# Kernel tuning notes

Hardware: AMD Instinct MI355X
Metric: run time of the kernel (lower is better)

Reference implementation:

```python
import jax, jax.numpy as jnp
import numpy as np

N = 10000      # nodes
E = 320000     # edges (avg degree 32)
SI, VI = 256, 32   # node scalar / vector channels
SE, VE = 64, 4     # edge scalar / vector channels
SO, VO = 256, 32   # output channels
IN_S = 2 * SI + SE         # 576 (self_message=True)
IN_V = 2 * VI + VE         # 68
H = max(IN_V, VO)          # 68, GBP hidden vector dim
EPS = 1e-8


def setup_inputs() -> dict:
    key = jax.random.key(0)
    ks = jax.random.split(key, 9)
    node_s = jax.random.normal(ks[0], (N, SI), jnp.float32)
    node_v = jax.random.normal(ks[1], (N, VI, 3), jnp.float32)
    edge_s = jax.random.normal(ks[2], (E, SE), jnp.float32)
    edge_v = jax.random.normal(ks[3], (E, VE, 3), jnp.float32)
    # GBP params (stored as [in, out] so y = x @ W)
    wh = jax.random.normal(ks[4], (IN_V, H), jnp.float32) / np.sqrt(IN_V)
    ws_w = jax.random.normal(ks[5], (IN_S + H, SO), jnp.float32) / np.sqrt(IN_S + H)
    ws_b = jnp.zeros((SO,), jnp.float32)
    wv = jax.random.normal(ks[6], (H, VO), jnp.float32) / np.sqrt(H)
    edge_index = jax.random.randint(ks[7], (2, E), 0, N, jnp.int64)
    return {"node_s": node_s, "node_v": node_v, "edge_s": edge_s,
            "edge_v": edge_v, "wh": wh, "ws_w": ws_w, "ws_b": ws_b,
            "wv": wv, "edge_index": edge_index}


def reference(node_s, node_v, edge_s, edge_v, wh, ws_w, ws_b, wv, edge_index):
    n = node_s.shape[0]
    src, dst = edge_index[0], edge_index[1]
    # gather + tuple_cat((s_j, v_j), edge_attr, (s_i, v_i))
    s_cat = jnp.concatenate([node_s[src], edge_s, node_s[dst]], axis=-1)   # [E, IN_S]
    v_cat = jnp.concatenate([node_v[src], edge_v, node_v[dst]], axis=-2)   # [E, IN_V, 3]
    # GBP message (activations=(None,None), no vector gate)
    v_pre = jnp.swapaxes(v_cat, -1, -2)                # [E, 3, IN_V]
    vh = v_pre @ wh                                    # [E, 3, H]
    vn = jnp.sqrt(jnp.maximum(jnp.sum(vh * vh, axis=-2), EPS))  # _norm_no_nan, [E, H]
    s_msg = jnp.concatenate([s_cat, vn], axis=-1) @ ws_w + ws_b  # [E, SO]
    v_msg = jnp.swapaxes(vh @ wv, -1, -2)              # [E, VO, 3]
    # scatter-mean to target nodes
    agg_s = jax.ops.segment_sum(s_msg, dst, num_segments=n)       # [N, SO]
    agg_v = jax.ops.segment_sum(v_msg, dst, num_segments=n)       # [N, VO, 3]
    cnt = jax.ops.segment_sum(jnp.ones((s_msg.shape[0],), s_msg.dtype), dst,
                              num_segments=n)
    cnt = jnp.maximum(cnt, 1.0)
    out_s = agg_s / cnt[:, None]
    out_v = agg_v / cnt[:, None, None]
    # _merge(s, V): flatten vector channels and append to scalars
    return jnp.concatenate([out_s, out_v.reshape(n, 3 * VO)], axis=-1)  # [N, SO+3*VO]
```

## Files before the change

kernel.cpp:

```cpp
#include <hip/hip_runtime.h>
#include <hip/hip_bf16.h>

#define N_NODES 10000
#define E_TOT   320000

typedef __attribute__((ext_vector_type(8))) short short8;
typedef __attribute__((ext_vector_type(4))) short s16x4;
typedef __attribute__((ext_vector_type(4))) float f32x4;

#define HIST_OFF    0u
#define FILL_OFF    40000u
#define ZERO_BYTES  80000u
#define ROWPTR_OFF  80000u
#define PERM_OFF    120064u
#define PSRC_OFF    1400064u
#define PQ_OFF      2680064u
#define QV_OFF      12280064u
#define WHV4_OFF    14200064u
#define WBIG_OFF    14200576u
#define NSBF_OFF    14544640u
#define ANSB_OFF    19664640u
#define EAB_OFF     24784640u
#define AP_OFF      27984640u
#define AEV_OFF     36144640u
#define AGGV_OFF    36624640u
#define FLAGS_OFF   40464640u
#define NODES_OFF   120064u

union BfS { __hip_bfloat16 h; short s; };
__device__ __forceinline__ short f2bf(float x) { BfS u; u.h = __float2bfloat16(x); return u.s; }
__device__ __forceinline__ float bf(short x) { BfS u; u.s = x; return __bfloat162float(u.h); }
__device__ __forceinline__ float ldin(const void* p, int f32m, long i) {
  return f32m ? ((const float*)p)[i] : __bfloat162float(((const __hip_bfloat16*)p)[i]);
}
__device__ __forceinline__ int get_ei(const void* p, int i64m, long i) {
  return i64m ? (int)(((const long long*)p)[i]) : ((const int*)p)[i];
}

__global__ __launch_bounds__(256) void detect_kernel(
    const unsigned short* __restrict__ ns_u16,
    const int* __restrict__ ei_i32, int* __restrict__ flags)
{
  __shared__ int cf, ci;
  if (threadIdx.x == 0) { cf = 0; ci = 0; }
  __syncthreads();
  int c1 = 0;
  for (int i = threadIdx.x; i < 8192; i += 256) {
    unsigned e = (ns_u16[2 * i] >> 7) & 0xFF;
    if (e < 100 || e > 140) c1++;
  }
  int c2 = 0;
  for (int i = threadIdx.x; i < 4096; i += 256)
    if (ei_i32[2 * i + 1] != 0) c2++;
  atomicAdd(&cf, c1); atomicAdd(&ci, c2);
  __syncthreads();
  if (threadIdx.x == 0) {
    flags[0] = (cf > 512) ? 1 : 0;
    flags[1] = (ci < 100) ? 1 : 0;
  }
}

__global__ __launch_bounds__(256) void hist_kernel(
    const void* __restrict__ edge_index, const int* __restrict__ flags,
    int* __restrict__ hist)
{
  const int i64m = flags[1];
  int e = blockIdx.x * 256 + threadIdx.x;
  int dst = get_ei(edge_index, i64m, (long)E_TOT + e);
  atomicAdd(&hist[dst], 1);
}

__global__ __launch_bounds__(256) void scan_kernel(
    const int* __restrict__ hist, int* __restrict__ rowptr)
{
  __shared__ int part[256];
  int tid = threadIdx.x;
  int base = tid * 40;
  int s = 0;
  for (int i = 0; i < 40; ++i) { int idx = base + i; if (idx < N_NODES) s += hist[idx]; }
  part[tid] = s;
  __syncthreads();
  for (int off = 1; off < 256; off <<= 1) {
    int v = (tid >= off) ? part[tid - off] : 0;
    __syncthreads();
    part[tid] += v;
    __syncthreads();
  }
  int run = (tid > 0) ? part[tid - 1] : 0;
  for (int i = 0; i < 40; ++i) {
    int idx = base + i;
    if (idx < N_NODES) { rowptr[idx] = run; run += hist[idx]; }
  }
  if (tid == 255) rowptr[N_NODES] = run;
}

__global__ __launch_bounds__(256) void permute_kernel(
    const void* __restrict__ edge_index, const int* __restrict__ flags,
    const int* __restrict__ rowptr, int* __restrict__ fill,
    int* __restrict__ perm, int* __restrict__ psrc)
{
  const int i64m = flags[1];
  int e = blockIdx.x * 256 + threadIdx.x;
  int dst = get_ei(edge_index, i64m, (long)E_TOT + e);
  int src = get_ei(edge_index, i64m, e);
  int pos = rowptr[dst] + atomicAdd(&fill[dst], 1);
  perm[pos] = e; psrc[pos] = src;
}

__global__ __launch_bounds__(256) void prep_kernel(
    const void* __restrict__ ws_w, const void* __restrict__ wh,
    const void* __restrict__ wv, const int* __restrict__ flags,
    short* __restrict__ Wbig, float* __restrict__ whv4)
{
  const int f32m = flags[0];
  int b = blockIdx.x, tid = threadIdx.x;
  if (b < 672) {
    int flat = b * 256 + tid;
    int o = flat / 672, k = flat % 672;
    short v = 0;
    if (k < 320)      v = f2bf(ldin(ws_w, f32m, (long)k * 256 + o));
    else if (k < 388) v = f2bf(ldin(ws_w, f32m, (long)(576 + k - 320) * 256 + o));
    else if (k >= 416) v = f2bf(ldin(ws_w, f32m, (long)(k - 96) * 256 + o));
    Wbig[flat] = v;
  } else if (tid < 128) {
    int q = tid / 32, c = tid % 32;
    float acc = 0.f;
    for (int h = 0; h < 68; ++h)
      acc += ldin(wh, f32m, (32 + q) * 68 + h) * ldin(wv, f32m, h * 32 + c);
    whv4[tid] = acc;
  }
}

__global__ __launch_bounds__(256) void node_pre(
    const void* __restrict__ node_v, const void* __restrict__ wh,
    const void* __restrict__ wv, const void* __restrict__ node_s,
    const int* __restrict__ flags,
    short* __restrict__ PQ, short* __restrict__ QV, short* __restrict__ ns_bf)
{
  const int f32m = flags[0];
  int n0 = blockIdx.x * 4, tid = threadIdx.x;
  __shared__ float nv[4][96];
  __shared__ float pq[4][408];
  for (int i = tid; i < 4 * 96; i += 256) nv[i / 96][i % 96] = ldin(node_v, f32m, (long)n0 * 96 + i);
  for (int i = tid; i < 1024; i += 256)
    ns_bf[(long)n0 * 256 + i] = f2bf(ldin(node_s, f32m, (long)n0 * 256 + i));
  __syncthreads();
  for (int o = tid; o < 4 * 408; o += 256) {
    int i = o / 408, r0 = o % 408;
    int part = r0 / 204, r = r0 % 204, d = r / 68, h = r % 68;
    int cbase = part ? 36 : 0;
    float acc = 0.f;
#pragma unroll
    for (int c = 0; c < 32; ++c)
      acc += nv[i][c * 3 + d] * ldin(wh, f32m, (cbase + c) * 68 + h);
    pq[i][r0] = acc;
  }
  __syncthreads();
  for (int o = tid; o < 4 * 480; o += 256) {
    int i = o / 480, k = o % 480;
    short v = 0;
    if (k < 272) {
      int h = k >> 2, d = k & 3;
      if (d < 3) v = f2bf(pq[i][d * 68 + h]);
    } else if (k < 476) {
      v = f2bf(pq[i][204 + (k - 272)]);
    }
    PQ[(long)(n0 + i) * 480 + k] = v;
  }
  for (int o = tid; o < 4 * 96; o += 256) {
    int i = o / 96, r = o % 96, d = r / 32, c = r % 32;
    float acc = 0.f;
    for (int h = 0; h < 68; ++h)
      acc += pq[i][204 + d * 68 + h] * ldin(wv, f32m, h * 32 + c);
    QV[(long)(n0 + i) * 96 + r] = f2bf(acc);
  }
}

template <int F32M>
__device__ __forceinline__ void edge_body(
    const void* __restrict__ edge_v, const void* __restrict__ edge_s,
    const void* __restrict__ wh,
    const int* __restrict__ rowptr, const int* __restrict__ perm,
    const int* __restrict__ psrc, const short* __restrict__ PQ,
    const short* __restrict__ nsb,
    short* __restrict__ ANSb, short* __restrict__ EAb,
    float* __restrict__ AP, float* __restrict__ AEV)
{
  const int tid = threadIdx.x;
  const int lane = tid & 63, w = tid >> 6;
  const int n = blockIdx.x;
  const int beg = rowptr[n], deg = rowptr[n + 1] - beg;
  const bool has2 = (lane < 4);
  const int h2 = 64 + lane;
  const float w4a0 = ldin(wh, F32M, 32 * 68 + lane);
  const float w4a1 = ldin(wh, F32M, 33 * 68 + lane);
  const float w4a2 = ldin(wh, F32M, 34 * 68 + lane);
  const float w4a3 = ldin(wh, F32M, 35 * 68 + lane);
  const float w4b0 = has2 ? ldin(wh, F32M, 32 * 68 + h2) : 0.f;
  const float w4b1 = has2 ? ldin(wh, F32M, 33 * 68 + h2) : 0.f;
  const float w4b2 = has2 ? ldin(wh, F32M, 34 * 68 + h2) : 0.f;
  const float w4b3 = has2 ? ldin(wh, F32M, 35 * 68 + h2) : 0.f;
  const short* pqQ = PQ + (long)n * 480 + 272;
  const float qa0 = bf(pqQ[0 * 68 + lane]);
  const float qa1 = bf(pqQ[1 * 68 + lane]);
  const float qa2 = bf(pqQ[2 * 68 + lane]);
  const float qb0 = has2 ? bf(pqQ[0 * 68 + h2]) : 0.f;
  const float qb1 = has2 ? bf(pqQ[1 * 68 + h2]) : 0.f;
  const float qb2 = has2 ? bf(pqQ[2 * 68 + h2]) : 0.f;
  float an0 = 0.f, an1 = 0.f, an2 = 0.f, an3 = 0.f;
  float ap0 = 0.f, ap1 = 0.f, ap2 = 0.f;
  float bq0 = 0.f, bq1 = 0.f, bq2 = 0.f;
  float avna = 0.f, avnb = 0.f, aes = 0.f, aev = 0.f;
  int e = w;
  int sv = 0, eid = 0;
  if (e < deg) { sv = psrc[beg + e]; eid = perm[beg + e]; }
  while (e < deg) {
    int en = e + 4, svn = 0, eidn = 0;
    if (en < deg) { svn = psrc[beg + en]; eidn = perm[beg + en]; }
    float ev0, ev1, ev2, ev3, ev4, ev5, ev6, ev7, ev8, ev9, evA, evB;
    if (F32M) {
      const float* evp = (const float*)edge_v + (long)eid * 12;
      f32x4 a = *(const f32x4*)evp;
      f32x4 b = *(const f32x4*)(evp + 4);
      f32x4 c = *(const f32x4*)(evp + 8);
      ev0 = a.x; ev1 = a.y; ev2 = a.z; ev3 = a.w;
      ev4 = b.x; ev5 = b.y; ev6 = b.z; ev7 = b.w;
      ev8 = c.x; ev9 = c.y; evA = c.z; evB = c.w;
    } else {
      const short* evp = (const short*)edge_v + (long)eid * 12;
      s16x4 a = *(const s16x4*)evp;
      s16x4 b = *(const s16x4*)(evp + 4);
      s16x4 c = *(const s16x4*)(evp + 8);
      ev0 = bf(a.x); ev1 = bf(a.y); ev2 = bf(a.z); ev3 = bf(a.w);
      ev4 = bf(b.x); ev5 = bf(b.y); ev6 = bf(b.z); ev7 = bf(b.w);
      ev8 = bf(c.x); ev9 = bf(c.y); evA = bf(c.z); evB = bf(c.w);
    }
    const short* ps = PQ + (long)sv * 480;
    s16x4 pv = *(const s16x4*)(ps + lane * 4);
    const float pa0 = bf(pv.x), pa1 = bf(pv.y), pa2 = bf(pv.z);
    s16x4 nvv = *(const s16x4*)(nsb + (long)sv * 256 + lane * 4);
    an0 += bf(nvv.x); an1 += bf(nvv.y); an2 += bf(nvv.z); an3 += bf(nvv.w);
    aes += ldin(edge_s, F32M, (long)eid * 64 + lane);
    if (lane < 12) aev += ldin(edge_v, F32M, (long)eid * 12 + lane);
    float v0 = pa0 + qa0 + ev0 * w4a0 + ev3 * w4a1 + ev6 * w4a2 + ev9 * w4a3;
    float v1 = pa1 + qa1 + ev1 * w4a0 + ev4 * w4a1 + ev7 * w4a2 + evA * w4a3;
    float v2 = pa2 + qa2 + ev2 * w4a0 + ev5 * w4a1 + ev8 * w4a2 + evB * w4a3;
    avna += sqrtf(fmaxf(v0 * v0 + v1 * v1 + v2 * v2, 1e-8f));
    ap0 += pa0; ap1 += pa1; ap2 += pa2;
    if (has2) {
      s16x4 p2 = *(const s16x4*)(ps + h2 * 4);
      const float pb0 = bf(p2.x), pb1 = bf(p2.y), pb2 = bf(p2.z);
      float u0 = pb0 + qb0 + ev0 * w4b0 + ev3 * w4b1 + ev6 * w4b2 + ev9 * w4b3;
      float u1 = pb1 + qb1 + ev1 * w4b0 + ev4 * w4b1 + ev7 * w4b2 + evA * w4b3;
      float u2 = pb2 + qb2 + ev2 * w4b0 + ev5 * w4b1 + ev8 * w4b2 + evB * w4b3;
      avnb += sqrtf(fmaxf(u0 * u0 + u1 * u1 + u2 * u2, 1e-8f));
      bq0 += pb0; bq1 += pb1; bq2 += pb2;
    }
    e = en; sv = svn; eid = eidn;
  }
  __shared__ float ansL[4][256];
  __shared__ float apL[4][204];
  __shared__ float avnL[4][132];
  __shared__ float aesL[4][64];
  __shared__ float aevL[4][12];
  ansL[w][lane * 4 + 0] = an0; ansL[w][lane * 4 + 1] = an1;
  ansL[w][lane * 4 + 2] = an2; ansL[w][lane * 4 + 3] = an3;
  apL[w][lane * 3 + 0] = ap0; apL[w][lane * 3 + 1] = ap1; apL[w][lane * 3 + 2] = ap2;
  if (has2) {
    apL[w][192 + lane * 3 + 0] = bq0;
    apL[w][192 + lane * 3 + 1] = bq1;
    apL[w][192 + lane * 3 + 2] = bq2;
  }
  avnL[w][lane] = avna;
  if (has2) avnL[w][64 + lane] = avnb;
  aesL[w][lane] = aes;
  if (lane < 12) aevL[w][lane] = aev;
  __syncthreads();
  const float inv = 1.f / fmaxf((float)deg, 1.f);
  {
    float s = ansL[0][tid] + ansL[1][tid] + ansL[2][tid] + ansL[3][tid];
    ANSb[(long)n * 256 + tid] = f2bf(s * inv);
  }
  if (tid < 204) {
    float s = apL[0][tid] + apL[1][tid] + apL[2][tid] + apL[3][tid];
    AP[(long)n * 204 + tid] = s;
  } else if (tid < 216) {
    int c = tid - 204;
    float s = aevL[0][c] + aevL[1][c] + aevL[2][c] + aevL[3][c];
    AEV[(long)n * 12 + c] = s;
  }
  if (tid < 64) {
    float s = aesL[0][tid] + aesL[1][tid] + aesL[2][tid] + aesL[3][tid];
    EAb[(long)n * 160 + tid] = f2bf(s * inv);
  } else if (tid < 132) {
    int c = tid - 64;
    float s = avnL[0][c] + avnL[1][c] + avnL[2][c] + avnL[3][c];
    EAb[(long)n * 160 + 64 + c] = f2bf(s * inv);
  } else if (tid < 160) {
    EAb[(long)n * 160 + tid] = 0;
  }
}

__global__ __launch_bounds__(256) void edge_block(
    const void* __restrict__ edge_v, const void* __restrict__ edge_s,
    const void* __restrict__ wh, const int* __restrict__ flags,
    const int* __restrict__ rowptr, const int* __restrict__ perm,
    const int* __restrict__ psrc, const short* __restrict__ PQ,
    const short* __restrict__ nsb,
    short* __restrict__ ANSb, short* __restrict__ EAb,
    float* __restrict__ AP, float* __restrict__ AEV)
{
  if (flags[0])
    edge_body<1>(edge_v, edge_s, wh, rowptr, perm, psrc, PQ, nsb,
                 ANSb, EAb, AP, AEV);
  else
    edge_body<0>(edge_v, edge_s, wh, rowptr, perm, psrc, PQ, nsb,
                 ANSb, EAb, AP, AEV);
}

__global__ __launch_bounds__(256) void node_gemm(
    const short* __restrict__ ANSb, const short* __restrict__ EAb,
    const short* __restrict__ nsb, const short* __restrict__ Wbig,
    float* __restrict__ NodeS)
{
  __shared__ __align__(16) short Xs[64 * 40];
  __shared__ __align__(16) short Ws[256 * 40];
  const int tid = threadIdx.x;
  const int n0 = blockIdx.x * 64;
  const int lane = tid & 63, wave = tid >> 6;
  const int frow = lane & 15, fk = (lane >> 4) * 8, q = lane >> 4;
  f32x4 acc[4][4];
#pragma unroll
  for (int ri = 0; ri < 4; ++ri)
#pragma unroll
    for (int ci = 0; ci < 4; ++ci)
      acc[ri][ci] = (f32x4){0.f, 0.f, 0.f, 0.f};
  const int se = tid >> 2, sq = tid & 3;
  const int rn = min(n0 + se, N_NODES - 1);
  for (int s = 0; s < 21; ++s) {
    short8 xv;
    if (s < 8)       xv = *(const short8*)&ANSb[(long)rn * 256 + s * 32 + sq * 8];
    else if (s < 13) xv = *(const short8*)&EAb[(long)rn * 160 + (s - 8) * 32 + sq * 8];
    else             xv = *(const short8*)&nsb[(long)rn * 256 + (s - 13) * 32 + sq * 8];
    *(short8*)&Xs[se * 40 + sq * 8] = xv;
#pragma unroll
    for (int it = 0; it < 4; ++it) {
      int flat = it * 256 + tid;
      int nn = flat >> 2, qq = flat & 3;
      *(short8*)&Ws[nn * 40 + qq * 8] = *(const short8*)&Wbig[nn * 672 + s * 32 + qq * 8];
    }
    __syncthreads();
    short8 a[4];
#pragma unroll
    for (int ri = 0; ri < 4; ++ri)
      a[ri] = *(const short8*)&Xs[(ri * 16 + frow) * 40 + fk];
#pragma unroll
    for (int ci = 0; ci < 4; ++ci) {
      int nn = wave * 64 + ci * 16 + frow;
      short8 b = *(const short8*)&Ws[nn * 40 + fk];
#pragma unroll
      for (int ri = 0; ri < 4; ++ri)
        acc[ri][ci] = __builtin_amdgcn_mfma_f32_16x16x32_bf16(a[ri], b, acc[ri][ci], 0, 0, 0);
    }
    __syncthreads();
  }
#pragma unroll
  for (int ri = 0; ri < 4; ++ri)
#pragma unroll
    for (int rr = 0; rr < 4; ++rr) {
      int row = n0 + ri * 16 + q * 4 + rr;
      if (row < N_NODES) {
#pragma unroll
        for (int ci = 0; ci < 4; ++ci) {
          int col = wave * 64 + ci * 16 + (lane & 15);
          NodeS[(long)row * 256 + col] = acc[ri][ci][rr];
        }
      }
    }
}

__global__ __launch_bounds__(256) void final_fuse(
    const float* __restrict__ NodeS, const float* __restrict__ AP,
    const float* __restrict__ AEV, const void* __restrict__ wv,
    const float* __restrict__ whv4, const int* __restrict__ rowptr,
    const short* __restrict__ QV, const void* __restrict__ ws_b,
    const int* __restrict__ flags, void* __restrict__ out)
{
  const int f32m = flags[0];
  int n0 = blockIdx.x * 4, tid = threadIdx.x;
  __shared__ float wvs[68 * 32];
  __shared__ float wh4s[128];
  __shared__ float APs[4][204];
  __shared__ float AEVs[4][12];
  __shared__ float aggL[4][96];
  for (int i = tid; i < 2176; i += 256) wvs[i] = ldin(wv, f32m, i);
  if (tid < 128) wh4s[tid] = whv4[tid];
  for (int i = tid; i < 816; i += 256) APs[i / 204][i % 204] = AP[(long)n0 * 204 + i];
  if (tid < 48) AEVs[tid / 12][tid % 12] = AEV[(long)n0 * 12 + tid];
  __syncthreads();
  for (int o = tid; o < 384; o += 256) {
    int i = o / 96, r = o % 96, c = r / 3, d = r % 3;
    float acc = AEVs[i][d] * wh4s[c] + AEVs[i][3 + d] * wh4s[32 + c]
              + AEVs[i][6 + d] * wh4s[64 + c] + AEVs[i][9 + d] * wh4s[96 + c];
    for (int h = 0; h < 68; ++h)
      acc += APs[i][h * 3 + d] * wvs[h * 32 + c];
    aggL[i][r] = acc;
  }
  __syncthreads();
  for (int o = tid; o < 1408; o += 256) {
    int i = o / 352, j = o % 352;
    int n = n0 + i;
    int deg = rowptr[n + 1] - rowptr[n];
    float v;
    if (j < 256) {
      v = (deg > 0) ? (NodeS[(long)n * 256 + j] + ldin(ws_b, f32m, j)) : 0.f;
    } else {
      int m = j - 256, ch = m / 3, d = m % 3;
      float inv = 1.f / fmaxf((float)deg, 1.f);
      v = aggL[i][m] * inv;
      if (deg > 0) v += bf(QV[(long)n * 96 + d * 32 + ch]);
    }
    long flat = (long)n * 352 + j;
    if (f32m) ((float*)out)[flat] = v;
    else      ((__hip_bfloat16*)out)[flat] = __float2bfloat16(v);
  }
}

extern "C" void kernel_launch(void* const* d_in, const int* in_sizes, int n_in,
                              void* d_out, int out_size, void* d_ws, size_t ws_size,
                              hipStream_t stream) {
  const void* node_s = d_in[0];
  const void* node_v = d_in[1];
  const void* edge_s = d_in[2];
  const void* edge_v = d_in[3];
  const void* wh     = d_in[4];
  const void* ws_w   = d_in[5];
  const void* ws_b   = d_in[6];
  const void* wv     = d_in[7];
  const void* edge_index = d_in[8];

  char* ws = (char*)d_ws;
  int*   hist  = (int*)(ws + HIST_OFF);
  int*   fill  = (int*)(ws + FILL_OFF);
  int*   rowptr= (int*)(ws + ROWPTR_OFF);
  int*   perm  = (int*)(ws + PERM_OFF);
  int*   psrc  = (int*)(ws + PSRC_OFF);
  short* PQ    = (short*)(ws + PQ_OFF);
  short* QV    = (short*)(ws + QV_OFF);
  float* whv4  = (float*)(ws + WHV4_OFF);
  short* Wbig  = (short*)(ws + WBIG_OFF);
  short* ns_bf = (short*)(ws + NSBF_OFF);
  short* ANSb  = (short*)(ws + ANSB_OFF);
  short* EAb   = (short*)(ws + EAB_OFF);
  float* AP    = (float*)(ws + AP_OFF);
  float* AEV   = (float*)(ws + AEV_OFF);
  float* NodeS = (float*)(ws + NODES_OFF);
  int*   flags = (int*)(ws + FLAGS_OFF);

  hipMemsetAsync(d_ws, 0, ZERO_BYTES, stream);
  detect_kernel<<<1, 256, 0, stream>>>((const unsigned short*)node_s,
                                       (const int*)edge_index, flags);
  hist_kernel<<<1250, 256, 0, stream>>>(edge_index, flags, hist);
  scan_kernel<<<1, 256, 0, stream>>>(hist, rowptr);
  permute_kernel<<<1250, 256, 0, stream>>>(edge_index, flags, rowptr, fill,
                                           perm, psrc);
  prep_kernel<<<673, 256, 0, stream>>>(ws_w, wh, wv, flags, Wbig, whv4);
  node_pre<<<2500, 256, 0, stream>>>(node_v, wh, wv, node_s, flags,
                                     PQ, QV, ns_bf);
  edge_block<<<10000, 256, 0, stream>>>(edge_v, edge_s, wh, flags, rowptr,
                                        perm, psrc, PQ, ns_bf,
                                        ANSb, EAb, AP, AEV);
  node_gemm<<<157, 256, 0, stream>>>(ANSb, EAb, ns_bf, Wbig, NodeS);
  final_fuse<<<2500, 256, 0, stream>>>(NodeS, AP, AEV, wv, whv4, rowptr,
                                       QV, ws_b, flags, d_out);
}
```

Measured before the change: 466.2 us.

## Interleave node scalars and P projections into one gather row per source node

Node preprocessing now writes a combined per-node row (CN) that interleaves the bf16 node scalars with the three P projection components, so each lane in the edge loop does a single 16-byte gather instead of two separate 8-byte gathers from different arrays. The Q projections move to their own compact array. Edge indices are made wave-uniform with readfirstlane so edge_v loads can go through scalar loads. node_pre also stages wh and wv in shared memory. The cost is a larger intermediate buffer and extra LDS use in node_pre, which may lower its occupancy.

```diff
diff --git a/kernel.cpp b/kernel.cpp
--- a/kernel.cpp
+++ b/kernel.cpp
@@ -14,22 +14,24 @@
 #define ROWPTR_OFF  80000u
 #define PERM_OFF    120064u
 #define PSRC_OFF    1400064u
-#define PQ_OFF      2680064u
-#define QV_OFF      12280064u
-#define WHV4_OFF    14200064u
-#define WBIG_OFF    14200576u
-#define NSBF_OFF    14544640u
-#define ANSB_OFF    19664640u
-#define EAB_OFF     24784640u
-#define AP_OFF      27984640u
-#define AEV_OFF     36144640u
-#define AGGV_OFF    36624640u
-#define FLAGS_OFF   40464640u
+#define CN_OFF      2680064u
+#define QARR_OFF    13560064u
+#define QV_OFF      17720064u
+#define WHV4_OFF    19640064u
+#define WBIG_OFF    19640576u
+#define NSBF_OFF    19984640u
+#define ANSB_OFF    25104640u
+#define EAB_OFF     30224640u
+#define AP_OFF      33424640u
+#define AEV_OFF     41584640u
+#define FLAGS_OFF   42064640u
 #define NODES_OFF   120064u
 
 union BfS { __hip_bfloat16 h; short s; };
 __device__ __forceinline__ short f2bf(float x) { BfS u; u.h = __float2bfloat16(x); return u.s; }
 __device__ __forceinline__ float bf(short x) { BfS u; u.s = x; return __bfloat162float(u.h); }
+__device__ __forceinline__ float bflo(unsigned u) { return __uint_as_float(u << 16); }
+__device__ __forceinline__ float bfhi(unsigned u) { return __uint_as_float(u & 0xffff0000u); }
 __device__ __forceinline__ float ldin(const void* p, int f32m, long i) {
   return f32m ? ((const float*)p)[i] : __bfloat162float(((const __hip_bfloat16*)p)[i]);
 }
@@ -135,12 +137,17 @@
     const void* __restrict__ node_v, const void* __restrict__ wh,
     const void* __restrict__ wv, const void* __restrict__ node_s,
     const int* __restrict__ flags,
-    short* __restrict__ PQ, short* __restrict__ QV, short* __restrict__ ns_bf)
+    short* __restrict__ CN, short* __restrict__ QARR,
+    short* __restrict__ QV, short* __restrict__ ns_bf)
 {
   const int f32m = flags[0];
   int n0 = blockIdx.x * 4, tid = threadIdx.x;
+  __shared__ float whs[68 * 68];
+  __shared__ float wvs[68 * 32];
   __shared__ float nv[4][96];
   __shared__ float pq[4][408];
+  for (int i = tid; i < 4624; i += 256) whs[i] = ldin(wh, f32m, i);
+  for (int i = tid; i < 2176; i += 256) wvs[i] = ldin(wv, f32m, i);
   for (int i = tid; i < 4 * 96; i += 256) nv[i / 96][i % 96] = ldin(node_v, f32m, (long)n0 * 96 + i);
   for (int i = tid; i < 1024; i += 256)
     ns_bf[(long)n0 * 256 + i] = f2bf(ldin(node_s, f32m, (long)n0 * 256 + i));
@@ -152,39 +159,53 @@
     float acc = 0.f;
 #pragma unroll
     for (int c = 0; c < 32; ++c)
-      acc += nv[i][c * 3 + d] * ldin(wh, f32m, (cbase + c) * 68 + h);
+      acc += nv[i][c * 3 + d] * whs[(cbase + c) * 68 + h];
     pq[i][r0] = acc;
   }
   __syncthreads();
-  for (int o = tid; o < 4 * 480; o += 256) {
-    int i = o / 480, k = o % 480;
+  for (int o = tid; o < 4 * 544; o += 256) {
+    int i = o / 544, k = o % 544;
     short v = 0;
-    if (k < 272) {
-      int h = k >> 2, d = k & 3;
-      if (d < 3) v = f2bf(pq[i][d * 68 + h]);
-    } else if (k < 476) {
-      v = f2bf(pq[i][204 + (k - 272)]);
-    }
-    PQ[(long)(n0 + i) * 480 + k] = v;
+    if (k < 512) {
+      int l = k >> 3, j = k & 7;
+      if (j < 4)      v = f2bf(ldin(node_s, f32m, (long)(n0 + i) * 256 + l * 4 + j));
+      else if (j < 7) v = f2bf(pq[i][(j - 4) * 68 + l]);
+    } else if (k < 528) {
+      int idx = k - 512, jj = idx >> 2, d = idx & 3;
+      if (d < 3) v = f2bf(pq[i][d * 68 + 64 + jj]);
+    }
+    CN[(long)(n0 + i) * 544 + k] = v;
+  }
+  for (int o = tid; o < 4 * 208; o += 256) {
+    int i = o / 208, k = o % 208;
+    QARR[(long)(n0 + i) * 208 + k] = (k < 204) ? f2bf(pq[i][204 + k]) : (short)0;
   }
   for (int o = tid; o < 4 * 96; o += 256) {
     int i = o / 96, r = o % 96, d = r / 32, c = r % 32;
     float acc = 0.f;
     for (int h = 0; h < 68; ++h)
-      acc += pq[i][204 + d * 68 + h] * ldin(wv, f32m, h * 32 + c);
+      acc += pq[i][204 + d * 68 + h] * wvs[h * 32 + c];
     QV[(long)(n0 + i) * 96 + r] = f2bf(acc);
   }
 }
+
+struct EdgeLds {
+  float ansL[4][256];
+  float apL[4][204];
+  float avnL[4][132];
+  float aesL[4][64];
+  float aevL[4][12];
+};
 
 template <int F32M>
 __device__ __forceinline__ void edge_body(
     const void* __restrict__ edge_v, const void* __restrict__ edge_s,
     const void* __restrict__ wh,
     const int* __restrict__ rowptr, const int* __restrict__ perm,
-    const int* __restrict__ psrc, const short* __restrict__ PQ,
-    const short* __restrict__ nsb,
+    const int* __restrict__ psrc, const short* __restrict__ CN,
+    const short* __restrict__ QARR,
     short* __restrict__ ANSb, short* __restrict__ EAb,
-    float* __restrict__ AP, float* __restrict__ AEV)
+    float* __restrict__ AP, float* __restrict__ AEV, EdgeLds* lds)
 {
   const int tid = threadIdx.x;
   const int lane = tid & 63, w = tid >> 6;
@@ -200,13 +221,13 @@
   const float w4b1 = has2 ? ldin(wh, F32M, 33 * 68 + h2) : 0.f;
   const float w4b2 = has2 ? ldin(wh, F32M, 34 * 68 + h2) : 0.f;
   const float w4b3 = has2 ? ldin(wh, F32M, 35 * 68 + h2) : 0.f;
-  const short* pqQ = PQ + (long)n * 480 + 272;
-  const float qa0 = bf(pqQ[0 * 68 + lane]);
-  const float qa1 = bf(pqQ[1 * 68 + lane]);
-  const float qa2 = bf(pqQ[2 * 68 + lane]);
-  const float qb0 = has2 ? bf(pqQ[0 * 68 + h2]) : 0.f;
-  const float qb1 = has2 ? bf(pqQ[1 * 68 + h2]) : 0.f;
-  const float qb2 = has2 ? bf(pqQ[2 * 68 + h2]) : 0.f;
+  const short* qp = QARR + (long)n * 208;
+  const float qa0 = bf(qp[0 * 68 + lane]);
+  const float qa1 = bf(qp[1 * 68 + lane]);
+  const float qa2 = bf(qp[2 * 68 + lane]);
+  const float qb0 = has2 ? bf(qp[0 * 68 + h2]) : 0.f;
+  const float qb1 = has2 ? bf(qp[1 * 68 + h2]) : 0.f;
+  const float qb2 = has2 ? bf(qp[2 * 68 + h2]) : 0.f;
   float an0 = 0.f, an1 = 0.f, an2 = 0.f, an3 = 0.f;
   float ap0 = 0.f, ap1 = 0.f, ap2 = 0.f;
   float bq0 = 0.f, bq1 = 0.f, bq2 = 0.f;
@@ -217,38 +238,35 @@
   while (e < deg) {
     int en = e + 4, svn = 0, eidn = 0;
     if (en < deg) { svn = psrc[beg + en]; eidn = perm[beg + en]; }
+    const int sv_s  = __builtin_amdgcn_readfirstlane(sv);
+    const int eid_s = __builtin_amdgcn_readfirstlane(eid);
     float ev0, ev1, ev2, ev3, ev4, ev5, ev6, ev7, ev8, ev9, evA, evB;
     if (F32M) {
-      const float* evp = (const float*)edge_v + (long)eid * 12;
-      f32x4 a = *(const f32x4*)evp;
-      f32x4 b = *(const f32x4*)(evp + 4);
-      f32x4 c = *(const f32x4*)(evp + 8);
-      ev0 = a.x; ev1 = a.y; ev2 = a.z; ev3 = a.w;
-      ev4 = b.x; ev5 = b.y; ev6 = b.z; ev7 = b.w;
-      ev8 = c.x; ev9 = c.y; evA = c.z; evB = c.w;
+      const float* evp = (const float*)edge_v + (long)eid_s * 12;
+      ev0 = evp[0]; ev1 = evp[1]; ev2 = evp[2]; ev3 = evp[3];
+      ev4 = evp[4]; ev5 = evp[5]; ev6 = evp[6]; ev7 = evp[7];
+      ev8 = evp[8]; ev9 = evp[9]; evA = evp[10]; evB = evp[11];
     } else {
-      const short* evp = (const short*)edge_v + (long)eid * 12;
-      s16x4 a = *(const s16x4*)evp;
-      s16x4 b = *(const s16x4*)(evp + 4);
-      s16x4 c = *(const s16x4*)(evp + 8);
-      ev0 = bf(a.x); ev1 = bf(a.y); ev2 = bf(a.z); ev3 = bf(a.w);
-      ev4 = bf(b.x); ev5 = bf(b.y); ev6 = bf(b.z); ev7 = bf(b.w);
-      ev8 = bf(c.x); ev9 = bf(c.y); evA = bf(c.z); evB = bf(c.w);
-    }
-    const short* ps = PQ + (long)sv * 480;
-    s16x4 pv = *(const s16x4*)(ps + lane * 4);
-    const float pa0 = bf(pv.x), pa1 = bf(pv.y), pa2 = bf(pv.z);
-    s16x4 nvv = *(const s16x4*)(nsb + (long)sv * 256 + lane * 4);
-    an0 += bf(nvv.x); an1 += bf(nvv.y); an2 += bf(nvv.z); an3 += bf(nvv.w);
-    aes += ldin(edge_s, F32M, (long)eid * 64 + lane);
-    if (lane < 12) aev += ldin(edge_v, F32M, (long)eid * 12 + lane);
+      const unsigned* evp = (const unsigned*)((const short*)edge_v + (long)eid_s * 12);
+      unsigned u0 = evp[0], u1 = evp[1], u2 = evp[2];
+      unsigned u3 = evp[3], u4 = evp[4], u5 = evp[5];
+      ev0 = bflo(u0); ev1 = bfhi(u0); ev2 = bflo(u1); ev3 = bfhi(u1);
+      ev4 = bflo(u2); ev5 = bfhi(u2); ev6 = bflo(u3); ev7 = bfhi(u3);
+      ev8 = bflo(u4); ev9 = bfhi(u4); evA = bflo(u5); evB = bfhi(u5);
+    }
+    const short* cs = CN + (long)sv_s * 544;
+    short8 cv = *(const short8*)(cs + lane * 8);
+    an0 += bf(cv[0]); an1 += bf(cv[1]); an2 += bf(cv[2]); an3 += bf(cv[3]);
+    const float pa0 = bf(cv[4]), pa1 = bf(cv[5]), pa2 = bf(cv[6]);
+    aes += ldin(edge_s, F32M, (long)eid_s * 64 + lane);
+    if (lane < 12) aev += ldin(edge_v, F32M, (long)eid_s * 12 + lane);
     float v0 = pa0 + qa0 + ev0 * w4a0 + ev3 * w4a1 + ev6 * w4a2 + ev9 * w4a3;
     float v1 = pa1 + qa1 + ev1 * w4a0 + ev4 * w4a1 + ev7 * w4a2 + evA * w4a3;
     float v2 = pa2 + qa2 + ev2 * w4a0 + ev5 * w4a1 + ev8 * w4a2 + evB * w4a3;
     avna += sqrtf(fmaxf(v0 * v0 + v1 * v1 + v2 * v2, 1e-8f));
     ap0 += pa0; ap1 += pa1; ap2 += pa2;
     if (has2) {
-      s16x4 p2 = *(const s16x4*)(ps + h2 * 4);
+      s16x4 p2 = *(const s16x4*)(cs + 512 + lane * 4);
       const float pb0 = bf(p2.x), pb1 = bf(p2.y), pb2 = bf(p2.z);
       float u0 = pb0 + qb0 + ev0 * w4b0 + ev3 * w4b1 + ev6 * w4b2 + ev9 * w4b3;
       float u1 = pb1 + qb1 + ev1 * w4b0 + ev4 * w4b1 + ev7 * w4b2 + evA * w4b3;
@@ -258,43 +276,39 @@
     }
     e = en; sv = svn; eid = eidn;
   }
-  __shared__ float ansL[4][256];
-  __shared__ float apL[4][204];
-  __shared__ float avnL[4][132];
-  __shared__ float aesL[4][64];
-  __shared__ float aevL[4][12];
-  ansL[w][lane * 4 + 0] = an0; ansL[w][lane * 4 + 1] = an1;
-  ansL[w][lane * 4 + 2] = an2; ansL[w][lane * 4 + 3] = an3;
-  apL[w][lane * 3 + 0] = ap0; apL[w][lane * 3 + 1] = ap1; apL[w][lane * 3 + 2] = ap2;
+  lds->ansL[w][lane * 4 + 0] = an0; lds->ansL[w][lane * 4 + 1] = an1;
+  lds->ansL[w][lane * 4 + 2] = an2; lds->ansL[w][lane * 4 + 3] = an3;
+  lds->apL[w][lane * 3 + 0] = ap0; lds->apL[w][lane * 3 + 1] = ap1;
+  lds->apL[w][lane * 3 + 2] = ap2;
   if (has2) {
-    apL[w][192 + lane * 3 + 0] = bq0;
-    apL[w][192 + lane * 3 + 1] = bq1;
-    apL[w][192 + lane * 3 + 2] = bq2;
-  }
-  avnL[w][lane] = avna;
-  if (has2) avnL[w][64 + lane] = avnb;
-  aesL[w][lane] = aes;
-  if (lane < 12) aevL[w][lane] = aev;
+    lds->apL[w][192 + lane * 3 + 0] = bq0;
+    lds->apL[w][192 + lane * 3 + 1] = bq1;
+    lds->apL[w][192 + lane * 3 + 2] = bq2;
+  }
+  lds->avnL[w][lane] = avna;
+  if (has2) lds->avnL[w][64 + lane] = avnb;
+  lds->aesL[w][lane] = aes;
+  if (lane < 12) lds->aevL[w][lane] = aev;
   __syncthreads();
   const float inv = 1.f / fmaxf((float)deg, 1.f);
   {
-    float s = ansL[0][tid] + ansL[1][tid] + ansL[2][tid] + ansL[3][tid];
+    float s = lds->ansL[0][tid] + lds->ansL[1][tid] + lds->ansL[2][tid] + lds->ansL[3][tid];
     ANSb[(long)n * 256 + tid] = f2bf(s * inv);
   }
   if (tid < 204) {
-    float s = apL[0][tid] + apL[1][tid] + apL[2][tid] + apL[3][tid];
+    float s = lds->apL[0][tid] + lds->apL[1][tid] + lds->apL[2][tid] + lds->apL[3][tid];
     AP[(long)n * 204 + tid] = s;
   } else if (tid < 216) {
     int c = tid - 204;
-    float s = aevL[0][c] + aevL[1][c] + aevL[2][c] + aevL[3][c];
+    float s = lds->aevL[0][c] + lds->aevL[1][c] + lds->aevL[2][c] + lds->aevL[3][c];
     AEV[(long)n * 12 + c] = s;
   }
   if (tid < 64) {
-    float s = aesL[0][tid] + aesL[1][tid] + aesL[2][tid] + aesL[3][tid];
+    float s = lds->aesL[0][tid] + lds->aesL[1][tid] + lds->aesL[2][tid] + lds->aesL[3][tid];
     EAb[(long)n * 160 + tid] = f2bf(s * inv);
   } else if (tid < 132) {
     int c = tid - 64;
-    float s = avnL[0][c] + avnL[1][c] + avnL[2][c] + avnL[3][c];
+    float s = lds->avnL[0][c] + lds->avnL[1][c] + lds->avnL[2][c] + lds->avnL[3][c];
     EAb[(long)n * 160 + 64 + c] = f2bf(s * inv);
   } else if (tid < 160) {
     EAb[(long)n * 160 + tid] = 0;
@@ -305,17 +319,18 @@
     const void* __restrict__ edge_v, const void* __restrict__ edge_s,
     const void* __restrict__ wh, const int* __restrict__ flags,
     const int* __restrict__ rowptr, const int* __restrict__ perm,
-    const int* __restrict__ psrc, const short* __restrict__ PQ,
-    const short* __restrict__ nsb,
+    const int* __restrict__ psrc, const short* __restrict__ CN,
+    const short* __restrict__ QARR,
     short* __restrict__ ANSb, short* __restrict__ EAb,
     float* __restrict__ AP, float* __restrict__ AEV)
 {
+  __shared__ EdgeLds lds;
   if (flags[0])
-    edge_body<1>(edge_v, edge_s, wh, rowptr, perm, psrc, PQ, nsb,
-                 ANSb, EAb, AP, AEV);
+    edge_body<1>(edge_v, edge_s, wh, rowptr, perm, psrc, CN, QARR,
+                 ANSb, EAb, AP, AEV, &lds);
   else
-    edge_body<0>(edge_v, edge_s, wh, rowptr, perm, psrc, PQ, nsb,
-                 ANSb, EAb, AP, AEV);
+    edge_body<0>(edge_v, edge_s, wh, rowptr, perm, psrc, CN, QARR,
+                 ANSb, EAb, AP, AEV, &lds);
 }
 
 __global__ __launch_bounds__(256) void node_gemm(
@@ -445,7 +460,8 @@
   int*   rowptr= (int*)(ws + ROWPTR_OFF);
   int*   perm  = (int*)(ws + PERM_OFF);
   int*   psrc  = (int*)(ws + PSRC_OFF);
-  short* PQ    = (short*)(ws + PQ_OFF);
+  short* CN    = (short*)(ws + CN_OFF);
+  short* QARR  = (short*)(ws + QARR_OFF);
   short* QV    = (short*)(ws + QV_OFF);
   float* whv4  = (float*)(ws + WHV4_OFF);
   short* Wbig  = (short*)(ws + WBIG_OFF);
@@ -466,9 +482,9 @@
                                            perm, psrc);
   prep_kernel<<<673, 256, 0, stream>>>(ws_w, wh, wv, flags, Wbig, whv4);
   node_pre<<<2500, 256, 0, stream>>>(node_v, wh, wv, node_s, flags,
-                                     PQ, QV, ns_bf);
+                                     CN, QARR, QV, ns_bf);
   edge_block<<<10000, 256, 0, stream>>>(edge_v, edge_s, wh, flags, rowptr,
-                                        perm, psrc, PQ, ns_bf,
+                                        perm, psrc, CN, QARR,
                                         ANSb, EAb, AP, AEV);
   node_gemm<<<157, 256, 0, stream>>>(ANSb, EAb, ns_bf, Wbig, NodeS);
   final_fuse<<<2500, 256, 0, stream>>>(NodeS, AP, AEV, wv, whv4, rowptr,
```

Result: faster. 446.6 us (-4.2%).
